# Kernel optimization log

Measured on AMD Instinct MI355X. Metric: run time of the kernel, lower is better.

Reference implementation:

```python
import jax, jax.numpy as jnp
import numpy as np

WS, SS, NH = 7, 3, 16  # window_size, shift_size, num_heads


def _rel_pos_index(ws):
    coords = np.stack(np.meshgrid(np.arange(ws), np.arange(ws), indexing='ij'))  # (2, ws, ws)
    cf = coords.reshape(2, -1)                       # (2, N)
    rel = (cf[:, :, None] - cf[:, None, :]).transpose(1, 2, 0).copy()  # (N, N, 2)
    rel[:, :, 0] += ws - 1
    rel[:, :, 1] += ws - 1
    rel[:, :, 0] *= 2 * ws - 1
    return rel.sum(-1)                               # (N, N) int indices into bias table


def _attn_mask(Hp, Wp, ws, ss):
    img = np.zeros((Hp, Wp))
    slices = (slice(0, -ws), slice(-ws, -ss), slice(-ss, None))
    cnt = 0
    for h in slices:
        for w in slices:
            img[h, w] = cnt
            cnt += 1
    mw = img.reshape(Hp // ws, ws, Wp // ws, ws).transpose(0, 2, 1, 3).reshape(-1, ws * ws)  # (nW, N)
    am = mw[:, None, :] - mw[:, :, None]             # (nW, N, N)
    return np.where(am != 0, -100.0, 0.0).astype(np.float32)


def setup_inputs() -> dict:
    key = jax.random.key(0)
    k1, k2, k3, k4 = jax.random.split(key, 4)
    B, H, W, C = 16, 56, 56, 512
    return {
        'q_out': jax.random.normal(k1, (B, H, W, C), dtype=jnp.float32),
        'k_out': jax.random.normal(k2, (B, H, W, C), dtype=jnp.float32),
        'v_out': jax.random.normal(k3, (B, H, W, C), dtype=jnp.float32),
        'bias_table': 0.02 * jax.random.normal(k4, ((2 * WS - 1) ** 2, NH), dtype=jnp.float32),
        'C': C, 'H': H, 'W': W,
        'x_low_padding_h': 0, 'x_low_padding_w': 0,
    }


def reference(q_out, k_out, v_out, bias_table, C, H, W, x_low_padding_h, x_low_padding_w):
    ws, ss, nh = WS, SS, NH
    Hp, Wp = H + x_low_padding_h, W + x_low_padding_w
    B = q_out.shape[0]
    hd = C // nh
    scale = hd ** (-0.5)
    N = ws * ws

    def part(x):  # (B,Hp,Wp,C) -> (B*nW, N, C)
        x = x.reshape(B, Hp // ws, ws, Wp // ws, ws, C).transpose(0, 1, 3, 2, 4, 5)
        return x.reshape(-1, N, C)

    # cyclic shift
    sq = jnp.roll(q_out, (-ss, -ss), axis=(1, 2))
    sk = jnp.roll(k_out, (-ss, -ss), axis=(1, 2))
    sv = jnp.roll(v_out, (-ss, -ss), axis=(1, 2))

    qw, kw, vw = part(sq), part(sk), part(sv)
    B_ = qw.shape[0]
    q = qw.reshape(B_, N, nh, hd).transpose(0, 2, 1, 3) * scale  # (B_, nh, N, hd)
    k = kw.reshape(B_, N, nh, hd).transpose(0, 2, 1, 3)
    v = vw.reshape(B_, N, nh, hd).transpose(0, 2, 1, 3)

    attn = jnp.einsum('bhnd,bhmd->bhnm', q, k)  # (B_, nh, N, N)

    # relative position bias
    rpi = _rel_pos_index(ws)
    bias = bias_table[rpi.reshape(-1)].reshape(N, N, nh).transpose(2, 0, 1)  # (nh, N, N)
    attn = attn + bias[None]

    # shift mask
    am = jnp.asarray(_attn_mask(Hp, Wp, ws, ss), dtype=attn.dtype)  # (nW, N, N)
    nW = am.shape[0]
    attn = attn.reshape(B_ // nW, nW, nh, N, N) + am[None, :, None]
    attn = jax.nn.softmax(attn.reshape(B_, nh, N, N), axis=-1)

    xw = jnp.einsum('bhnm,bhmd->bhnd', attn, v).transpose(0, 2, 1, 3).reshape(B_, N, C)

    # window reverse + reverse shift
    x = xw.reshape(B, Hp // ws, Wp // ws, ws, ws, C).transpose(0, 1, 3, 2, 4, 5).reshape(B, Hp, Wp, C)
    return jnp.roll(x, (ss, ss), axis=(1, 2))
```

## Files before the change

kernel.cpp:

```cpp
#include <hip/hip_runtime.h>
#include <stdint.h>


constexpr int WSZ  = 7;
constexpr int NTOK = 49;
constexpr int NH_  = 16;
constexpr int HD_  = 32;
constexpr int SP   = 56;
constexpr int CH   = 512;
constexpr float LOG2E = 1.4426950408889634f;

typedef float  f32x4 __attribute__((ext_vector_type(4)));
typedef short  s16x8 __attribute__((ext_vector_type(8)));

union FragU { uint32_t w[4]; s16x8 v; };

__device__ inline uint32_t bf16_hibits(float x) {
    uint32_t u = __float_as_uint(x);
    u += 0x7fffu + ((u >> 16) & 1u);
    return u & 0xffff0000u;
}

__device__ inline uint32_t pk_bf16(float a, float b) {
    return (bf16_hibits(a) >> 16) | bf16_hibits(b);
}

__device__ inline void hilo_pair(float a, float b, uint32_t& wh, uint32_t& wl) {
    uint32_t ah = bf16_hibits(a), bh = bf16_hibits(b);
    wh = (ah >> 16) | bh;
    float ra = a - __uint_as_float(ah);
    float rb = b - __uint_as_float(bh);
    wl = pk_bf16(ra, rb);
}

__global__ __launch_bounds__(256)
void build_bm(const float* __restrict__ bias, float* __restrict__ bm)
{
    const int blk = blockIdx.x;
    const int h = blk >> 2, cls = blk & 3;
    for (int idx = threadIdx.x; idx < 4096; idx += 256) {
        const int q = idx >> 6, m = idx & 63;
        float val;
        if (q >= NTOK || m >= NTOK) {
            val = -1e9f;
        } else {
            const int iq = q / 7, jq = q % 7, im = m / 7, jm = m % 7;
            const int rpi = (iq - im + 6) * 13 + (jq - jm + 6);
            const float bv = bias[rpi * NH_ + h];
            const int rq = ((cls & 2) ? (iq < 4 ? 3 : 6) : 0)
                         + ((cls & 1) ? (jq < 4 ? 1 : 2) : 0);
            const int rm = ((cls & 2) ? (im < 4 ? 3 : 6) : 0)
                         + ((cls & 1) ? (jm < 4 ? 1 : 2) : 0);
            const float mask = (rq != rm) ? -100.0f : 0.0f;
            val = (bv + mask) * LOG2E - 23.0f;
        }
        bm[blk * 4096 + idx] = val;
    }
}

__global__ __launch_bounds__(256, 2)
void swin_mfma_kernel(const float* __restrict__ qg,
                      const float* __restrict__ kg,
                      const float* __restrict__ vg,
                      const float* __restrict__ bm,
                      float* __restrict__ outg)
{
    const int wave = threadIdx.x >> 6;
    const int wh   = blockIdx.x * 4 + wave;
    const int h    = wh & (NH_ - 1);
    const int w    = wh >> 4;
    const int wc   = w & 7;
    const int wr   = (w >> 3) & 7;
    const int b    = w >> 6;

    const int lane = threadIdx.x & 63;
    const int g    = lane >> 4;
    const int l16  = lane & 15;

    const int t  = lane < NTOK ? lane : NTOK - 1;
    const int it = t / 7, jt = t - 7 * it;
    int sr = wr * 7 + it + 3; if (sr >= SP) sr -= SP;
    int sc = wc * 7 + jt + 3; if (sc >= SP) sc -= SP;
    const int off_t = ((b * SP + sr) * SP + sc) * CH + h * HD_;

    int oQK[4];
#pragma unroll
    for (int tt = 0; tt < 4; ++tt)
        oQK[tt] = __shfl(off_t, 16 * tt + l16);
    int oV[16];
#pragma unroll
    for (int mc = 0; mc < 2; ++mc)
#pragma unroll
        for (int e = 0; e < 8; ++e)
            oV[8 * mc + e] = __shfl(off_t, 32 * mc + 8 * g + e);

    float4 qa[4][2], ka[4][2];
#pragma unroll
    for (int tt = 0; tt < 4; ++tt) {
        const float* qp = qg + oQK[tt] + 8 * g;
        const float* kp = kg + oQK[tt] + 8 * g;
        qa[tt][0] = *(const float4*)qp;
        qa[tt][1] = *(const float4*)(qp + 4);
        ka[tt][0] = *(const float4*)kp;
        ka[tt][1] = *(const float4*)(kp + 4);
    }
    float va[2][2][8];
#pragma unroll
    for (int mc = 0; mc < 2; ++mc)
#pragma unroll
        for (int dh = 0; dh < 2; ++dh)
#pragma unroll
            for (int e = 0; e < 8; ++e)
                va[mc][dh][e] = vg[oV[8 * mc + e] + 16 * dh + l16];

    const float qs = 0.17677669529663687f * LOG2E;

    s16x8 Qh[4], Kh[4], Kl[4];
#pragma unroll
    for (int tt = 0; tt < 4; ++tt) {
        FragU qh, kh, kl;
        qh.w[0] = pk_bf16(qa[tt][0].x * qs, qa[tt][0].y * qs);
        qh.w[1] = pk_bf16(qa[tt][0].z * qs, qa[tt][0].w * qs);
        qh.w[2] = pk_bf16(qa[tt][1].x * qs, qa[tt][1].y * qs);
        qh.w[3] = pk_bf16(qa[tt][1].z * qs, qa[tt][1].w * qs);
        hilo_pair(ka[tt][0].x, ka[tt][0].y, kh.w[0], kl.w[0]);
        hilo_pair(ka[tt][0].z, ka[tt][0].w, kh.w[1], kl.w[1]);
        hilo_pair(ka[tt][1].x, ka[tt][1].y, kh.w[2], kl.w[2]);
        hilo_pair(ka[tt][1].z, ka[tt][1].w, kh.w[3], kl.w[3]);
        Qh[tt] = qh.v; Kh[tt] = kh.v; Kl[tt] = kl.v;
    }
    s16x8 Vb[2][2];
#pragma unroll
    for (int mc = 0; mc < 2; ++mc)
#pragma unroll
        for (int dh = 0; dh < 2; ++dh) {
            FragU fu;
#pragma unroll
            for (int wd = 0; wd < 4; ++wd)
                fu.w[wd] = pk_bf16(va[mc][dh][2 * wd], va[mc][dh][2 * wd + 1]);
            Vb[mc][dh] = fu.v;
        }

    const int cls = ((wr == 7) ? 2 : 0) | ((wc == 7) ? 1 : 0);
    const float* bmh = bm + (h * 4 + cls) * 4096;

    uint32_t u0[4][4], u1[4][4];
    float inv[4];
#pragma unroll
    for (int tq = 0; tq < 4; ++tq) {
        float dsum = 0.f;
#pragma unroll
        for (int tk = 0; tk < 4; ++tk) {
            f32x4 a = *(const f32x4*)(bmh + (16 * tq + l16) * 64 + 16 * tk + 4 * g);
            a = __builtin_amdgcn_mfma_f32_16x16x32_bf16(Kl[tk], Qh[tq], a, 0, 0, 0);
            a = __builtin_amdgcn_mfma_f32_16x16x32_bf16(Kh[tk], Qh[tq], a, 0, 0, 0);
            float e0 = __builtin_amdgcn_exp2f(a[0]);
            float e1 = __builtin_amdgcn_exp2f(a[1]);
            float e2 = __builtin_amdgcn_exp2f(a[2]);
            float e3 = __builtin_amdgcn_exp2f(a[3]);
            dsum += (e0 + e1) + (e2 + e3);
            u0[tq][tk] = pk_bf16(e0, e1);
            u1[tq][tk] = pk_bf16(e2, e3);
        }
        dsum += __shfl_xor(dsum, 16);
        dsum += __shfl_xor(dsum, 32);
        inv[tq] = 1.0f / (dsum + 1e-30f);
    }

    const int srcb = 32 * (g & 1) + l16;
    const bool hiG = (lane >= 32);
    s16x8 PA[4][2];
#pragma unroll
    for (int tq = 0; tq < 4; ++tq)
#pragma unroll
        for (int mc = 0; mc < 2; ++mc) {
            FragU fu;
#pragma unroll
            for (int wd = 0; wd < 4; ++wd) {
                const int sl = srcb + 16 * (wd >> 1);
                uint32_t A, B;
                if (wd & 1) {
                    A = __shfl(u1[tq][2 * mc],     sl);
                    B = __shfl(u1[tq][2 * mc + 1], sl);
                } else {
                    A = __shfl(u0[tq][2 * mc],     sl);
                    B = __shfl(u0[tq][2 * mc + 1], sl);
                }
                fu.w[wd] = hiG ? B : A;
            }
            PA[tq][mc] = fu.v;
        }

#pragma unroll
    for (int tq = 0; tq < 4; ++tq) {
        f32x4 acc[2];
#pragma unroll
        for (int dh = 0; dh < 2; ++dh) {
            f32x4 a = {0.f, 0.f, 0.f, 0.f};
            a = __builtin_amdgcn_mfma_f32_16x16x32_bf16(PA[tq][0], Vb[0][dh], a, 0, 0, 0);
            a = __builtin_amdgcn_mfma_f32_16x16x32_bf16(PA[tq][1], Vb[1][dh], a, 0, 0, 0);
            acc[dh] = a;
        }
#pragma unroll
        for (int r = 0; r < 4; ++r) {
            const float iv = __shfl(inv[tq], 4 * g + r);
            const int oo = __shfl(off_t, 16 * tq + 4 * g + r);
            if (tq < 3 || (g == 0 && r == 0)) {
#pragma unroll
                for (int dh = 0; dh < 2; ++dh)
                    outg[oo + 16 * dh + l16] = acc[dh][r] * iv;
            }
        }
    }
}

__global__ __launch_bounds__(256)
void swin_block_scalar(const float* __restrict__ qg,
                       const float* __restrict__ kg,
                       const float* __restrict__ vg,
                       const float* __restrict__ bias,
                       float* __restrict__ outg)
{
    const int wave = __builtin_amdgcn_readfirstlane(threadIdx.x >> 6);
    const int wh   = blockIdx.x * 4 + wave;
    const int h    = wh & (NH_ - 1);
    const int w    = wh >> 4;
    const int wc   = w & 7;
    const int wr   = (w >> 3) & 7;
    const int b    = w >> 6;

    const int lane = threadIdx.x & 63;
    const int rr   = lane < NTOK ? lane : NTOK - 1;
    const int i    = rr / WSZ;
    const int j    = rr - i * WSZ;

    const int hp = wr * WSZ + i;
    const int wp = wc * WSZ + j;
    int sr = hp + 3; if (sr >= SP) sr -= SP;
    int sc = wp + 3; if (sc >= SP) sc -= SP;
    const int rowoff = ((b * SP + sr) * SP + sc) * CH + h * HD_;
    const int reg_r = (hp < 49 ? 0 : (hp < 53 ? 3 : 6))
                    + (wp < 49 ? 0 : (wp < 53 ? 1 : 2));
    const float qscale = 0.17677669529663687f * LOG2E;

    float qr[HD_];
    {
        const float4* qp = reinterpret_cast<const float4*>(qg + rowoff);
#pragma unroll
        for (int tt = 0; tt < HD_ / 4; ++tt) {
            float4 x = qp[tt];
            qr[4*tt+0] = x.x * qscale; qr[4*tt+1] = x.y * qscale;
            qr[4*tt+2] = x.z * qscale; qr[4*tt+3] = x.w * qscale;
        }
    }
    const int biaslane = (i * 13 + j) * 16 + h;
    float o[HD_];
#pragma unroll
    for (int d = 0; d < HD_; ++d) o[d] = 0.f;
    float denom = 0.f;
    const float* kb = kg + b * SP * SP * CH + h * HD_;
    const float* vb = vg + b * SP * SP * CH + h * HD_;

    for (int ic = 0; ic < WSZ; ++ic) {
        const int hpc = wr * WSZ + ic;
        int src_r = hpc + 3; if (src_r >= SP) src_r -= SP;
        const int regh_c = (hpc < 49 ? 0 : (hpc < 53 ? 3 : 6));
        const float* krow0 = kb + src_r * SP * CH;
        const float* vrow0 = vb + src_r * SP * CH;
        float e[WSZ];
#pragma unroll
        for (int u = 0; u < WSZ; ++u) {
            const int wpc = wc * WSZ + u;
            int src_c = wpc + 3; if (src_c >= SP) src_c -= SP;
            const int reg_c = regh_c + (wpc < 49 ? 0 : (wpc < 53 ? 1 : 2));
            const float* krow = krow0 + src_c * CH;
            const float bv = bias[biaslane + ((6 - ic) * 13 + (6 - u)) * 16];
            float s0 = fmaf(bv, LOG2E, (reg_r != reg_c) ? -167.26950408889634f : -23.0f);
            float s1 = 0.f, s2 = 0.f, s3 = 0.f;
#pragma unroll
            for (int d = 0; d < HD_; d += 4) {
                s0 = fmaf(qr[d+0], krow[d+0], s0);
                s1 = fmaf(qr[d+1], krow[d+1], s1);
                s2 = fmaf(qr[d+2], krow[d+2], s2);
                s3 = fmaf(qr[d+3], krow[d+3], s3);
            }
            e[u] = exp2f((s0 + s1) + (s2 + s3));
            denom += e[u];
        }
#pragma unroll
        for (int u = 0; u < WSZ; ++u) {
            const int wpc = wc * WSZ + u;
            int src_c = wpc + 3; if (src_c >= SP) src_c -= SP;
            const float* vrow = vrow0 + src_c * CH;
            const float ev = e[u];
#pragma unroll
            for (int d = 0; d < HD_; ++d) o[d] = fmaf(ev, vrow[d], o[d]);
        }
    }
    const float invd = 1.0f / denom;
    if (lane < NTOK) {
        float4* op = reinterpret_cast<float4*>(outg + rowoff);
#pragma unroll
        for (int tt = 0; tt < HD_ / 4; ++tt) {
            float4 x;
            x.x = o[4*tt+0] * invd; x.y = o[4*tt+1] * invd;
            x.z = o[4*tt+2] * invd; x.w = o[4*tt+3] * invd;
            op[tt] = x;
        }
    }
}

extern "C" void kernel_launch(void* const* d_in, const int* in_sizes, int n_in,
                              void* d_out, int out_size, void* d_ws, size_t ws_size,
                              hipStream_t stream) {
    const float* q    = (const float*)d_in[0];
    const float* k    = (const float*)d_in[1];
    const float* v    = (const float*)d_in[2];
    const float* bias = (const float*)d_in[3];
    float* out        = (float*)d_out;

    const int B   = in_sizes[0] / (SP * SP * CH);
    const int nwh = B * (SP / WSZ) * (SP / WSZ) * NH_;

    const size_t bm_bytes = (size_t)NH_ * 4 * 64 * 64 * sizeof(float);
    if (ws_size >= bm_bytes) {
        float* bm = (float*)d_ws;
        hipLaunchKernelGGL(build_bm, dim3(NH_ * 4), dim3(256), 0, stream, bias, bm);
        hipLaunchKernelGGL(swin_mfma_kernel, dim3(nwh / 4), dim3(256), 0, stream,
                           q, k, v, bm, out);
    } else {
        hipLaunchKernelGGL(swin_block_scalar, dim3(nwh / 4), dim3(256), 0, stream,
                           q, k, v, bias, out);
    }
}
```

Before: 118.4 us.

## Process one window per block and stage K/V as bf16 in LDS

The kernel now launches one 1024-thread block per window, with one wave per head. Each wave loads whole K and V token rows as coalesced float4 reads, converts them to bf16 (hi/lo split for K), and writes them to LDS. After a block barrier, each head wave builds its MFMA fragments from LDS, which replaces the strided per-head global loads, in particular the scalar gather of V. The cost is about 150 KB of LDS per block, which allows only one block per CU, adds a block-wide sync, and stages load, convert and compute in sequence with little overlap.

```diff
diff --git a/kernel.cpp b/kernel.cpp
--- a/kernel.cpp
+++ b/kernel.cpp
@@ -10,6 +10,9 @@
 constexpr int CH   = 512;
 constexpr float LOG2E = 1.4426950408889634f;
 
+constexpr int LDSTRIDE = 520;
+constexpr size_t LDS_BYTES = (size_t)3 * NTOK * LDSTRIDE * 2;
+
 typedef float  f32x4 __attribute__((ext_vector_type(4)));
 typedef short  s16x8 __attribute__((ext_vector_type(8)));
 
@@ -20,11 +23,9 @@
     u += 0x7fffu + ((u >> 16) & 1u);
     return u & 0xffff0000u;
 }
-
 __device__ inline uint32_t pk_bf16(float a, float b) {
     return (bf16_hibits(a) >> 16) | bf16_hibits(b);
 }
-
 __device__ inline void hilo_pair(float a, float b, uint32_t& wh, uint32_t& wl) {
     uint32_t ah = bf16_hibits(a), bh = bf16_hibits(b);
     wh = (ah >> 16) | bh;
@@ -58,24 +59,45 @@
     }
 }
 
-__global__ __launch_bounds__(256, 2)
-void swin_mfma_kernel(const float* __restrict__ qg,
-                      const float* __restrict__ kg,
-                      const float* __restrict__ vg,
-                      const float* __restrict__ bm,
-                      float* __restrict__ outg)
+__global__ __launch_bounds__(1024, 4)
+void swin_window_kernel(const float* __restrict__ qg,
+                        const float* __restrict__ kg,
+                        const float* __restrict__ vg,
+                        const float* __restrict__ bm,
+                        float* __restrict__ outg)
 {
-    const int wave = threadIdx.x >> 6;
-    const int wh   = blockIdx.x * 4 + wave;
-    const int h    = wh & (NH_ - 1);
-    const int w    = wh >> 4;
+    extern __shared__ unsigned short smem[];
+    unsigned short* KhL = smem;
+    unsigned short* KlL = smem + NTOK * LDSTRIDE;
+    unsigned short* VL  = smem + 2 * NTOK * LDSTRIDE;
+
+    const int w    = blockIdx.x;
     const int wc   = w & 7;
     const int wr   = (w >> 3) & 7;
     const int b    = w >> 6;
-
+    const int wave = threadIdx.x >> 6;
+    const int h    = wave;
     const int lane = threadIdx.x & 63;
     const int g    = lane >> 4;
     const int l16  = lane & 15;
+
+    float4 kst[4][2], vst[4][2];
+#pragma unroll
+    for (int s = 0; s < 4; ++s) {
+        const int r = wave + 16 * s;
+        if (r < NTOK) {
+            const int i = r / 7, j = r - 7 * i;
+            int srow = wr * 7 + i + 3; if (srow >= SP) srow -= SP;
+            int scol = wc * 7 + j + 3; if (scol >= SP) scol -= SP;
+            const int ro = ((b * SP + srow) * SP + scol) * CH + 8 * lane;
+            const float* kp = kg + ro;
+            const float* vp = vg + ro;
+            kst[s][0] = *(const float4*)kp;
+            kst[s][1] = *(const float4*)(kp + 4);
+            vst[s][0] = *(const float4*)vp;
+            vst[s][1] = *(const float4*)(vp + 4);
+        }
+    }
 
     const int t  = lane < NTOK ? lane : NTOK - 1;
     const int it = t / 7, jt = t - 7 * it;
@@ -87,59 +109,56 @@
 #pragma unroll
     for (int tt = 0; tt < 4; ++tt)
         oQK[tt] = __shfl(off_t, 16 * tt + l16);
-    int oV[16];
-#pragma unroll
-    for (int mc = 0; mc < 2; ++mc)
-#pragma unroll
-        for (int e = 0; e < 8; ++e)
-            oV[8 * mc + e] = __shfl(off_t, 32 * mc + 8 * g + e);
-
-    float4 qa[4][2], ka[4][2];
+
+    float4 qa[4][2];
 #pragma unroll
     for (int tt = 0; tt < 4; ++tt) {
         const float* qp = qg + oQK[tt] + 8 * g;
-        const float* kp = kg + oQK[tt] + 8 * g;
         qa[tt][0] = *(const float4*)qp;
         qa[tt][1] = *(const float4*)(qp + 4);
-        ka[tt][0] = *(const float4*)kp;
-        ka[tt][1] = *(const float4*)(kp + 4);
-    }
-    float va[2][2][8];
-#pragma unroll
-    for (int mc = 0; mc < 2; ++mc)
-#pragma unroll
-        for (int dh = 0; dh < 2; ++dh)
-#pragma unroll
-            for (int e = 0; e < 8; ++e)
-                va[mc][dh][e] = vg[oV[8 * mc + e] + 16 * dh + l16];
+    }
+
+#pragma unroll
+    for (int s = 0; s < 4; ++s) {
+        const int r = wave + 16 * s;
+        if (r < NTOK) {
+            FragU kh, kl, vb;
+            hilo_pair(kst[s][0].x, kst[s][0].y, kh.w[0], kl.w[0]);
+            hilo_pair(kst[s][0].z, kst[s][0].w, kh.w[1], kl.w[1]);
+            hilo_pair(kst[s][1].x, kst[s][1].y, kh.w[2], kl.w[2]);
+            hilo_pair(kst[s][1].z, kst[s][1].w, kh.w[3], kl.w[3]);
+            vb.w[0] = pk_bf16(vst[s][0].x, vst[s][0].y);
+            vb.w[1] = pk_bf16(vst[s][0].z, vst[s][0].w);
+            vb.w[2] = pk_bf16(vst[s][1].x, vst[s][1].y);
+            vb.w[3] = pk_bf16(vst[s][1].z, vst[s][1].w);
+            *(s16x8*)(KhL + r * LDSTRIDE + 8 * lane) = kh.v;
+            *(s16x8*)(KlL + r * LDSTRIDE + 8 * lane) = kl.v;
+            *(s16x8*)(VL  + r * LDSTRIDE + 8 * lane) = vb.v;
+        }
+    }
 
     const float qs = 0.17677669529663687f * LOG2E;
-
-    s16x8 Qh[4], Kh[4], Kl[4];
+    s16x8 Qh[4];
 #pragma unroll
     for (int tt = 0; tt < 4; ++tt) {
-        FragU qh, kh, kl;
+        FragU qh;
         qh.w[0] = pk_bf16(qa[tt][0].x * qs, qa[tt][0].y * qs);
         qh.w[1] = pk_bf16(qa[tt][0].z * qs, qa[tt][0].w * qs);
         qh.w[2] = pk_bf16(qa[tt][1].x * qs, qa[tt][1].y * qs);
         qh.w[3] = pk_bf16(qa[tt][1].z * qs, qa[tt][1].w * qs);
-        hilo_pair(ka[tt][0].x, ka[tt][0].y, kh.w[0], kl.w[0]);
-        hilo_pair(ka[tt][0].z, ka[tt][0].w, kh.w[1], kl.w[1]);
-        hilo_pair(ka[tt][1].x, ka[tt][1].y, kh.w[2], kl.w[2]);
-        hilo_pair(ka[tt][1].z, ka[tt][1].w, kh.w[3], kl.w[3]);
-        Qh[tt] = qh.v; Kh[tt] = kh.v; Kl[tt] = kl.v;
-    }
-    s16x8 Vb[2][2];
-#pragma unroll
-    for (int mc = 0; mc < 2; ++mc)
-#pragma unroll
-        for (int dh = 0; dh < 2; ++dh) {
-            FragU fu;
-#pragma unroll
-            for (int wd = 0; wd < 4; ++wd)
-                fu.w[wd] = pk_bf16(va[mc][dh][2 * wd], va[mc][dh][2 * wd + 1]);
-            Vb[mc][dh] = fu.v;
-        }
+        Qh[tt] = qh.v;
+    }
+
+    __syncthreads();
+
+    s16x8 Kh[4], Kl[4];
+#pragma unroll
+    for (int tt = 0; tt < 4; ++tt) {
+        int row = 16 * tt + l16; if (row > NTOK - 1) row = NTOK - 1;
+        const int o = row * LDSTRIDE + h * HD_ + 8 * g;
+        Kh[tt] = *(const s16x8*)(KhL + o);
+        Kl[tt] = *(const s16x8*)(KlL + o);
+    }
 
     const int cls = ((wr == 7) ? 2 : 0) | ((wc == 7) ? 1 : 0);
     const float* bmh = bm + (h * 4 + cls) * 4096;
@@ -166,6 +185,26 @@
         dsum += __shfl_xor(dsum, 32);
         inv[tq] = 1.0f / (dsum + 1e-30f);
     }
+
+    s16x8 Vb[2][2];
+#pragma unroll
+    for (int mc = 0; mc < 2; ++mc)
+#pragma unroll
+        for (int dh = 0; dh < 2; ++dh) {
+            FragU fu;
+#pragma unroll
+            for (int wd = 0; wd < 4; ++wd) {
+                int r0 = 32 * mc + 8 * g + 2 * wd;
+                int r1 = r0 + 1;
+                if (r0 > NTOK - 1) r0 = NTOK - 1;
+                if (r1 > NTOK - 1) r1 = NTOK - 1;
+                const int co = h * HD_ + 16 * dh + l16;
+                const uint32_t lo = VL[r0 * LDSTRIDE + co];
+                const uint32_t hi = VL[r1 * LDSTRIDE + co];
+                fu.w[wd] = lo | (hi << 16);
+            }
+            Vb[mc][dh] = fu.v;
+        }
 
     const int srcb = 32 * (g & 1) + l16;
     const bool hiG = (lane >= 32);
@@ -319,17 +358,20 @@
     const float* bias = (const float*)d_in[3];
     float* out        = (float*)d_out;
 
-    const int B   = in_sizes[0] / (SP * SP * CH);
-    const int nwh = B * (SP / WSZ) * (SP / WSZ) * NH_;
+    const int B  = in_sizes[0] / (SP * SP * CH);
+    const int nW = B * (SP / WSZ) * (SP / WSZ);
 
     const size_t bm_bytes = (size_t)NH_ * 4 * 64 * 64 * sizeof(float);
     if (ws_size >= bm_bytes) {
         float* bm = (float*)d_ws;
+        (void)hipFuncSetAttribute(
+            reinterpret_cast<const void*>(swin_window_kernel),
+            hipFuncAttributeMaxDynamicSharedMemorySize, (int)LDS_BYTES);
         hipLaunchKernelGGL(build_bm, dim3(NH_ * 4), dim3(256), 0, stream, bias, bm);
-        hipLaunchKernelGGL(swin_mfma_kernel, dim3(nwh / 4), dim3(256), 0, stream,
+        hipLaunchKernelGGL(swin_window_kernel, dim3(nW), dim3(1024), LDS_BYTES, stream,
                            q, k, v, bm, out);
     } else {
-        hipLaunchKernelGGL(swin_block_scalar, dim3(nwh / 4), dim3(256), 0, stream,
+        hipLaunchKernelGGL(swin_block_scalar, dim3(nW * NH_ / 4), dim3(256), 0, stream,
                            q, k, v, bias, out);
     }
 }
```

Result: slower. 124.4 us (+5.1%).

## Drop K hi/lo split, store bias-mask table as fp16, vectorize output stores

Applied to the files above, without the earlier changes.

Removes the K low-part bf16 MFMA, so QK^T runs as a single bf16 MFMA per tile instead of two. The bias+mask table is stored in fp16 and prefetched into registers before a scheduling barrier, which halves its memory traffic. The PV MFMA operands are swapped so each lane holds contiguous output channels, allowing float4 stores and removing the per-row shuffles of the normalizer and offsets. The trade is lower precision in the QK^T logits and the bias values.

```diff
diff --git a/kernel.cpp b/kernel.cpp
--- a/kernel.cpp
+++ b/kernel.cpp
@@ -10,31 +10,23 @@
 constexpr int CH   = 512;
 constexpr float LOG2E = 1.4426950408889634f;
 
-typedef float  f32x4 __attribute__((ext_vector_type(4)));
-typedef short  s16x8 __attribute__((ext_vector_type(8)));
+typedef float    f32x4 __attribute__((ext_vector_type(4)));
+typedef short    s16x8 __attribute__((ext_vector_type(8)));
+typedef _Float16 f16x4 __attribute__((ext_vector_type(4)));
 
 union FragU { uint32_t w[4]; s16x8 v; };
 
-__device__ inline uint32_t bf16_hibits(float x) {
+__device__ __forceinline__ uint32_t bf16_hibits(float x) {
     uint32_t u = __float_as_uint(x);
     u += 0x7fffu + ((u >> 16) & 1u);
     return u & 0xffff0000u;
 }
-
-__device__ inline uint32_t pk_bf16(float a, float b) {
+__device__ __forceinline__ uint32_t pk_bf16(float a, float b) {
     return (bf16_hibits(a) >> 16) | bf16_hibits(b);
 }
 
-__device__ inline void hilo_pair(float a, float b, uint32_t& wh, uint32_t& wl) {
-    uint32_t ah = bf16_hibits(a), bh = bf16_hibits(b);
-    wh = (ah >> 16) | bh;
-    float ra = a - __uint_as_float(ah);
-    float rb = b - __uint_as_float(bh);
-    wl = pk_bf16(ra, rb);
-}
-
 __global__ __launch_bounds__(256)
-void build_bm(const float* __restrict__ bias, float* __restrict__ bm)
+void build_bm(const float* __restrict__ bias, _Float16* __restrict__ bm)
 {
     const int blk = blockIdx.x;
     const int h = blk >> 2, cls = blk & 3;
@@ -42,7 +34,7 @@
         const int q = idx >> 6, m = idx & 63;
         float val;
         if (q >= NTOK || m >= NTOK) {
-            val = -1e9f;
+            val = -1000.0f;
         } else {
             const int iq = q / 7, jq = q % 7, im = m / 7, jm = m % 7;
             const int rpi = (iq - im + 6) * 13 + (jq - jm + 6);
@@ -52,9 +44,9 @@
             const int rm = ((cls & 2) ? (im < 4 ? 3 : 6) : 0)
                          + ((cls & 1) ? (jm < 4 ? 1 : 2) : 0);
             const float mask = (rq != rm) ? -100.0f : 0.0f;
-            val = (bv + mask) * LOG2E - 23.0f;
-        }
-        bm[blk * 4096 + idx] = val;
+            val = (bv + mask) * LOG2E;
+        }
+        bm[blk * 4096 + idx] = (_Float16)val;
     }
 }
 
@@ -62,7 +54,7 @@
 void swin_mfma_kernel(const float* __restrict__ qg,
                       const float* __restrict__ kg,
                       const float* __restrict__ vg,
-                      const float* __restrict__ bm,
+                      const _Float16* __restrict__ bm,
                       float* __restrict__ outg)
 {
     const int wave = threadIdx.x >> 6;
@@ -85,24 +77,23 @@
 
     int oQK[4];
 #pragma unroll
-    for (int tt = 0; tt < 4; ++tt)
-        oQK[tt] = __shfl(off_t, 16 * tt + l16);
+    for (int tt = 0; tt < 4; ++tt) oQK[tt] = __shfl(off_t, 16 * tt + l16);
     int oV[16];
 #pragma unroll
     for (int mc = 0; mc < 2; ++mc)
 #pragma unroll
-        for (int e = 0; e < 8; ++e)
-            oV[8 * mc + e] = __shfl(off_t, 32 * mc + 8 * g + e);
+        for (int e = 0; e < 8; ++e) oV[8 * mc + e] = __shfl(off_t, 32 * mc + 8 * g + e);
+
+    const int cls = ((wr == 7) ? 2 : 0) | ((wc == 7) ? 1 : 0);
+    const _Float16* bmh = bm + ((size_t)h * 4 + cls) * 4096;
 
     float4 qa[4][2], ka[4][2];
 #pragma unroll
     for (int tt = 0; tt < 4; ++tt) {
         const float* qp = qg + oQK[tt] + 8 * g;
         const float* kp = kg + oQK[tt] + 8 * g;
-        qa[tt][0] = *(const float4*)qp;
-        qa[tt][1] = *(const float4*)(qp + 4);
-        ka[tt][0] = *(const float4*)kp;
-        ka[tt][1] = *(const float4*)(kp + 4);
+        qa[tt][0] = *(const float4*)qp;  qa[tt][1] = *(const float4*)(qp + 4);
+        ka[tt][0] = *(const float4*)kp;  ka[tt][1] = *(const float4*)(kp + 4);
     }
     float va[2][2][8];
 #pragma unroll
@@ -112,24 +103,31 @@
 #pragma unroll
             for (int e = 0; e < 8; ++e)
                 va[mc][dh][e] = vg[oV[8 * mc + e] + 16 * dh + l16];
+    f16x4 bmr[4][4];
+#pragma unroll
+    for (int tq = 0; tq < 4; ++tq)
+#pragma unroll
+        for (int tk = 0; tk < 4; ++tk)
+            bmr[tq][tk] = *(const f16x4*)(bmh + (16 * tq + l16) * 64 + 16 * tk + 4 * g);
+
+    __builtin_amdgcn_sched_barrier(0);
 
     const float qs = 0.17677669529663687f * LOG2E;
 
-    s16x8 Qh[4], Kh[4], Kl[4];
+    s16x8 Qh[4], Kh[4], Vb[2][2];
 #pragma unroll
     for (int tt = 0; tt < 4; ++tt) {
-        FragU qh, kh, kl;
+        FragU qh, kh;
         qh.w[0] = pk_bf16(qa[tt][0].x * qs, qa[tt][0].y * qs);
         qh.w[1] = pk_bf16(qa[tt][0].z * qs, qa[tt][0].w * qs);
         qh.w[2] = pk_bf16(qa[tt][1].x * qs, qa[tt][1].y * qs);
         qh.w[3] = pk_bf16(qa[tt][1].z * qs, qa[tt][1].w * qs);
-        hilo_pair(ka[tt][0].x, ka[tt][0].y, kh.w[0], kl.w[0]);
-        hilo_pair(ka[tt][0].z, ka[tt][0].w, kh.w[1], kl.w[1]);
-        hilo_pair(ka[tt][1].x, ka[tt][1].y, kh.w[2], kl.w[2]);
-        hilo_pair(ka[tt][1].z, ka[tt][1].w, kh.w[3], kl.w[3]);
-        Qh[tt] = qh.v; Kh[tt] = kh.v; Kl[tt] = kl.v;
-    }
-    s16x8 Vb[2][2];
+        kh.w[0] = pk_bf16(ka[tt][0].x, ka[tt][0].y);
+        kh.w[1] = pk_bf16(ka[tt][0].z, ka[tt][0].w);
+        kh.w[2] = pk_bf16(ka[tt][1].x, ka[tt][1].y);
+        kh.w[3] = pk_bf16(ka[tt][1].z, ka[tt][1].w);
+        Qh[tt] = qh.v; Kh[tt] = kh.v;
+    }
 #pragma unroll
     for (int mc = 0; mc < 2; ++mc)
 #pragma unroll
@@ -141,9 +139,6 @@
             Vb[mc][dh] = fu.v;
         }
 
-    const int cls = ((wr == 7) ? 2 : 0) | ((wc == 7) ? 1 : 0);
-    const float* bmh = bm + (h * 4 + cls) * 4096;
-
     uint32_t u0[4][4], u1[4][4];
     float inv[4];
 #pragma unroll
@@ -151,8 +146,11 @@
         float dsum = 0.f;
 #pragma unroll
         for (int tk = 0; tk < 4; ++tk) {
-            f32x4 a = *(const f32x4*)(bmh + (16 * tq + l16) * 64 + 16 * tk + 4 * g);
-            a = __builtin_amdgcn_mfma_f32_16x16x32_bf16(Kl[tk], Qh[tq], a, 0, 0, 0);
+            f32x4 a;
+            a[0] = (float)bmr[tq][tk][0] - 23.f;
+            a[1] = (float)bmr[tq][tk][1] - 23.f;
+            a[2] = (float)bmr[tq][tk][2] - 23.f;
+            a[3] = (float)bmr[tq][tk][3] - 23.f;
             a = __builtin_amdgcn_mfma_f32_16x16x32_bf16(Kh[tk], Qh[tq], a, 0, 0, 0);
             float e0 = __builtin_amdgcn_exp2f(a[0]);
             float e1 = __builtin_amdgcn_exp2f(a[1]);
@@ -193,22 +191,18 @@
 
 #pragma unroll
     for (int tq = 0; tq < 4; ++tq) {
-        f32x4 acc[2];
+        const float iv = inv[tq];
+        const bool ok = (tq < 3) || (l16 == 0);
 #pragma unroll
         for (int dh = 0; dh < 2; ++dh) {
             f32x4 a = {0.f, 0.f, 0.f, 0.f};
-            a = __builtin_amdgcn_mfma_f32_16x16x32_bf16(PA[tq][0], Vb[0][dh], a, 0, 0, 0);
-            a = __builtin_amdgcn_mfma_f32_16x16x32_bf16(PA[tq][1], Vb[1][dh], a, 0, 0, 0);
-            acc[dh] = a;
-        }
-#pragma unroll
-        for (int r = 0; r < 4; ++r) {
-            const float iv = __shfl(inv[tq], 4 * g + r);
-            const int oo = __shfl(off_t, 16 * tq + 4 * g + r);
-            if (tq < 3 || (g == 0 && r == 0)) {
-#pragma unroll
-                for (int dh = 0; dh < 2; ++dh)
-                    outg[oo + 16 * dh + l16] = acc[dh][r] * iv;
+            a = __builtin_amdgcn_mfma_f32_16x16x32_bf16(Vb[0][dh], PA[tq][0], a, 0, 0, 0);
+            a = __builtin_amdgcn_mfma_f32_16x16x32_bf16(Vb[1][dh], PA[tq][1], a, 0, 0, 0);
+            if (ok) {
+                float4 st;
+                st.x = a[0] * iv; st.y = a[1] * iv;
+                st.z = a[2] * iv; st.w = a[3] * iv;
+                *(float4*)(outg + oQK[tq] + 16 * dh + 4 * g) = st;
             }
         }
     }
@@ -322,9 +316,9 @@
     const int B   = in_sizes[0] / (SP * SP * CH);
     const int nwh = B * (SP / WSZ) * (SP / WSZ) * NH_;
 
-    const size_t bm_bytes = (size_t)NH_ * 4 * 64 * 64 * sizeof(float);
+    const size_t bm_bytes = (size_t)NH_ * 4 * 4096 * sizeof(_Float16);
     if (ws_size >= bm_bytes) {
-        float* bm = (float*)d_ws;
+        _Float16* bm = (_Float16*)d_ws;
         hipLaunchKernelGGL(build_bm, dim3(NH_ * 4), dim3(256), 0, stream, bias, bm);
         hipLaunchKernelGGL(swin_mfma_kernel, dim3(nwh / 4), dim3(256), 0, stream,
                            q, k, v, bm, out);
```

Result: slower. 121.2 us (+2.4%).
